# Kernel tuning notes

Hardware: AMD Instinct MI355X
Metric: run time of the kernel (lower is better)

Reference implementation:

```python
import jax, jax.numpy as jnp
import numpy as np

B, H, W, C1, C2 = 4, 256, 256, 256, 128
K = 128   # cells per patch (fixed for jit; original uses torch.unique)
E = 256   # emb_dim
NC = 16   # n_classes
G = 512   # n_genes
R = 64    # n_ref
HEADS = 8


def _w(k, shape):
    return jax.random.normal(k, shape, jnp.float32) / np.float32(np.sqrt(shape[-2]))


def setup_inputs() -> dict:
    key = jax.random.key(0)
    ks = jax.random.split(key, 20)
    return {
        "hd1": jax.random.normal(ks[0], (B, C1, H, W), jnp.float32),
        "h1": jax.random.normal(ks[1], (B, C2, H, W), jnp.float32),
        "ref_orig": jax.random.uniform(ks[2], (R, G), jnp.float32),
        "embed_w": _w(ks[3], (2 * (C1 + C2), E)),
        "comp_w1": _w(ks[4], (E, E)), "comp_w2": _w(ks[5], (E, NC)),
        "hist_w1": _w(ks[6], (E, E)), "hist_w2": _w(ks[7], (E, NC)),
        "genes_w1": _w(ks[8], (G, E)), "genes_w2": _w(ks[9], (E, NC)),
        "wref_w1": _w(ks[10], (3, E, E)), "wref_w2": _w(ks[11], (3, E, R)),
        "ca_wq": _w(ks[12], (3, NC, E)), "ca_wk": _w(ks[13], (3, G, E)),
        "ca_wv": _w(ks[14], (3, G, E)), "ca_wo": _w(ks[15], (3, E, G)),
        "nuclei_mask": jax.random.randint(ks[16], (B, H, W), 0, K + 1, jnp.int32),
        "n_cells": K,
    }


def _forward(hd1, h1, ref_orig, embed_w, comp_w1, comp_w2, hist_w1, hist_w2,
             genes_w1, genes_w2, wref_w1, wref_w2, ca_wq, ca_wk, ca_wv, ca_wo,
             nuclei_mask, n_cells):
    b, c1, hgt, wid = hd1.shape
    k_cells = n_cells
    # replaces the per-cell mask-multiply-sum loop with one segment reduce
    feat = jnp.concatenate([hd1, h1], axis=1)            # [B, C1+C2, H, W]
    cf = feat.shape[1]
    feat_flat = feat.transpose(0, 2, 3, 1).reshape(b * hgt * wid, cf)
    ids = nuclei_mask.reshape(b, hgt * wid)
    seg = jnp.where(ids > 0, jnp.arange(b)[:, None] * k_cells + ids - 1,
                    b * k_cells).reshape(-1)
    nseg = b * k_cells + 1                               # last bucket = background
    sums = jax.ops.segment_sum(feat_flat, seg, num_segments=nseg)[: b * k_cells]
    area = jax.ops.segment_sum(jnp.ones((seg.shape[0],), feat.dtype), seg,
                               num_segments=nseg)[: b * k_cells]
    cell_feat = sums / jnp.maximum(area, 1.0)[:, None]   # [N, Cf]
    glob = feat.mean((2, 3))                             # [B, Cf] = fv_hd1 ++ fv_h1
    all_fv = jnp.concatenate([cell_feat, jnp.repeat(glob, k_cells, axis=0)], axis=1)
    emb = all_fv @ embed_w                               # [N, E]
    emb_patches = emb.reshape(b, k_cells, -1).mean(1)    # per-patch mean embedding
    comp = jax.nn.softmax(jax.nn.relu(emb_patches @ comp_w1) @ comp_w2, axis=-1)
    comp_tiled = jnp.repeat(comp, k_cells, axis=0)       # [N, NC]
    out_cell_type = jax.nn.relu(emb @ hist_w1) @ hist_w2

    def branch(w1, w2, wq, wk, wv, wo):
        rw = jax.nn.softmax(jax.nn.relu(emb @ w1) @ w2, axis=-1)   # [N, R]
        ref_weighted = rw @ ref_orig                               # [N, G]
        dh = wq.shape[1] // HEADS
        q = (comp_tiled @ wq).reshape(-1, HEADS, dh)
        k = (ref_weighted @ wk).reshape(-1, HEADS, dh)
        v = (ref_weighted @ wv).reshape(-1, HEADS, dh)
        attn = jax.nn.softmax(jnp.einsum("qhd,khd->hqk", q, k) / float(np.sqrt(dh)), axis=-1)
        o = jnp.einsum("hqk,khd->qhd", attn, v).reshape(-1, HEADS * dh)
        return jax.nn.relu(ref_weighted + o @ wo)

    out_exprs = jax.vmap(branch)(wref_w1, wref_w2, ca_wq, ca_wk, ca_wv, ca_wo)  # [3,N,G]
    genes_h = jax.nn.relu(out_exprs[0] @ genes_w1)
    out_cell_type_expr = genes_h @ genes_w2
    return out_cell_type, out_exprs, out_cell_type_expr, genes_h, comp, area


def reference(hd1, h1, ref_orig, embed_w, comp_w1, comp_w2, hist_w1, hist_w2,
              genes_w1, genes_w2, wref_w1, wref_w2, ca_wq, ca_wk, ca_wv, ca_wo,
              nuclei_mask, n_cells):
    out_cell_type, out_exprs, out_cell_type_expr, genes_h, comp, area = _forward(
        hd1, h1, ref_orig, embed_w, comp_w1, comp_w2, hist_w1, hist_w2,
        genes_w1, genes_w2, wref_w1, wref_w2, ca_wq, ca_wk, ca_wv, ca_wo,
        nuclei_mask, n_cells)
    return (out_cell_type, out_exprs[0], out_exprs[1], out_exprs[2],
            out_cell_type_expr, genes_h, comp, area)
```

## Files before the change

kernel.cpp:

```cpp
#include <hip/hip_runtime.h>
#include <hip/hip_bf16.h>

#define Bn 4
#define C1n 256
#define C2n 128
#define CF 384
#define HWn 65536
#define Kc 128
#define Nn 512
#define En 256
#define NCn 16
#define Gn 512
#define Rn 64
#define HEADSn 8
#define DHn 32

#define CHK 16
#define PCH2 (HWn/CHK)
#define TC2 32
#define NT 64

#define SCALE_F 1048576.0f
#define INV_SCALE (1.0f/1048576.0f)

typedef unsigned long long ull;

__global__ void zero_k(ull* __restrict__ p, int n) {
    int i = blockIdx.x * 256 + threadIdx.x;
    if (i < n) p[i] = 0ULL;
}

__global__ __launch_bounds__(256) void area_k(const int* __restrict__ mask,
                                              int* __restrict__ area_i32) {
    int chunk = blockIdx.x, b = blockIdx.y;
    __shared__ int hist[4][129];
    int t = threadIdx.x, w = t >> 6;
    for (int i = t; i < 4 * 129; i += 256) ((int*)hist)[i] = 0;
    __syncthreads();
    const int* mp = mask + (size_t)b * HWn + chunk * PCH2;
    #pragma unroll
    for (int it = 0; it < 4; ++it) {
        int4 v = *(const int4*)(mp + it * 1024 + t * 4);
        atomicAdd(&hist[w][v.x], 1);
        atomicAdd(&hist[w][v.y], 1);
        atomicAdd(&hist[w][v.z], 1);
        atomicAdd(&hist[w][v.w], 1);
    }
    __syncthreads();
    if (t < 128) {
        int tot = hist[0][t+1] + hist[1][t+1] + hist[2][t+1] + hist[3][t+1];
        if (tot) atomicAdd(&area_i32[b * Kc + t], tot);
    }
}

__global__ __launch_bounds__(256) void segreduce3_k(
        const float* __restrict__ hd1, const float* __restrict__ h1,
        const int* __restrict__ mask,
        ull* __restrict__ sums64, ull* __restrict__ bg64) {
    int chunk = blockIdx.x, cg = blockIdx.y, b = blockIdx.z;
    int c0 = cg * TC2;
    const float* base = (c0 < C1n)
        ? hd1 + ((size_t)(b * C1n + c0)) * HWn
        : h1  + ((size_t)(b * C2n + (c0 - C1n))) * HWn;
    const int* mp = mask + (size_t)b * HWn + chunk * PCH2;

    __shared__ ull bins64[129 * TC2];
    __shared__ float tile[NT * 33];
    __shared__ __align__(16) int idsh[NT];

    int t = threadIdx.x;
    int cL = t >> 3, l8 = t & 7;
    int cA = t & 31, pg = t >> 5;
    for (int i = t; i < 129 * TC2; i += 256) bins64[i] = 0ULL;
    __syncthreads();

    for (int tl = 0; tl < PCH2 / NT; ++tl) {
        int px0 = tl * NT;
        float4 v0 = *(const float4*)(base + (size_t)cL * HWn + px0 + l8 * 4);
        float4 v1 = *(const float4*)(base + (size_t)cL * HWn + px0 + 32 + l8 * 4);
        if (t < 16) *(int4*)&idsh[t * 4] = *(const int4*)(mp + px0 + t * 4);
        int p0 = l8 * 4;
        tile[(p0 + 0) * 33 + cL] = v0.x;
        tile[(p0 + 1) * 33 + cL] = v0.y;
        tile[(p0 + 2) * 33 + cL] = v0.z;
        tile[(p0 + 3) * 33 + cL] = v0.w;
        tile[(32 + p0 + 0) * 33 + cL] = v1.x;
        tile[(32 + p0 + 1) * 33 + cL] = v1.y;
        tile[(32 + p0 + 2) * 33 + cL] = v1.z;
        tile[(32 + p0 + 3) * 33 + cL] = v1.w;
        __syncthreads();
        #pragma unroll
        for (int pp = 0; pp < 8; ++pp) {
            int p = pg * 8 + pp;
            int id = idsh[p];
            float v = tile[p * 33 + cA];
            long long qv = __float2ll_rn(v * SCALE_F);
            atomicAdd(&bins64[id * TC2 + cA], (ull)qv);
        }
        __syncthreads();
    }
    for (int i = t; i < 129 * TC2; i += 256) {
        int cell = i >> 5, cc = i & 31;
        ull v = bins64[i];
        if (v) {
            if (cell == 0) atomicAdd(&bg64[b * CF + c0 + cc], v);
            else atomicAdd(&sums64[((size_t)(b * Kc + cell - 1)) * CF + c0 + cc], v);
        }
    }
}

__global__ void glob_k(const ull* __restrict__ sums64, const ull* __restrict__ bg64,
                       const int* __restrict__ area_i32, float* __restrict__ glob,
                       float* __restrict__ areaf, float* __restrict__ area_out) {
    int idx = blockIdx.x * 256 + threadIdx.x;
    if (idx < Bn * CF) {
        int b = idx / CF, c = idx - b * CF;
        long long s = (long long)bg64[idx];
        for (int cell = 0; cell < Kc; ++cell)
            s += (long long)sums64[((size_t)(b * Kc + cell)) * CF + c];
        glob[idx] = (float)s * (INV_SCALE / (float)HWn);
    }
    if (idx < Nn) {
        float a = (float)area_i32[idx];
        areaf[idx] = a;
        area_out[idx] = a;
    }
}

__global__ __launch_bounds__(256) void gemm_emb_k(
        const ull* __restrict__ sums64, const float* __restrict__ glob,
        const float* __restrict__ areaf, const float* __restrict__ Bw,
        float* __restrict__ C) {
    int row0 = blockIdx.x * 2;
    __shared__ float As[2 * 768];
    __shared__ float part[2048];
    __shared__ float rina[2];
    int t = threadIdx.x, lane = t & 63, w = t >> 6;
    if (t < 2) rina[t] = 1.f / fmaxf(areaf[row0 + t], 1.f);
    __syncthreads();
    for (int idx = t; idx < 2 * 768; idx += 256) {
        int r = idx / 768, k = idx - r * 768;
        int row = row0 + r;
        float v;
        if (k < CF) v = (float)(long long)sums64[(size_t)row * CF + k] * INV_SCALE * rina[r];
        else        v = glob[(row >> 7) * CF + (k - CF)];
        As[idx] = v;
    }
    __syncthreads();
    float acc[2][4] = {{0,0,0,0},{0,0,0,0}};
    const int KQ = 192;
    const float* bp = Bw + (size_t)(w * KQ) * 256 + lane * 4;
    #pragma unroll 8
    for (int k = 0; k < KQ; ++k) {
        float4 bv = *(const float4*)(bp + (size_t)k * 256);
        float a0 = As[w * KQ + k], a1 = As[768 + w * KQ + k];
        acc[0][0] = fmaf(a0, bv.x, acc[0][0]); acc[0][1] = fmaf(a0, bv.y, acc[0][1]);
        acc[0][2] = fmaf(a0, bv.z, acc[0][2]); acc[0][3] = fmaf(a0, bv.w, acc[0][3]);
        acc[1][0] = fmaf(a1, bv.x, acc[1][0]); acc[1][1] = fmaf(a1, bv.y, acc[1][1]);
        acc[1][2] = fmaf(a1, bv.z, acc[1][2]); acc[1][3] = fmaf(a1, bv.w, acc[1][3]);
    }
    *(float4*)&part[(w * 2 + 0) * 256 + lane * 4] = make_float4(acc[0][0], acc[0][1], acc[0][2], acc[0][3]);
    *(float4*)&part[(w * 2 + 1) * 256 + lane * 4] = make_float4(acc[1][0], acc[1][1], acc[1][2], acc[1][3]);
    __syncthreads();
    #pragma unroll
    for (int i2 = 0; i2 < 2; ++i2) {
        int idx = i2 * 256 + t, r = idx >> 8, c = idx & 255;
        float s = part[r*256+c] + part[(2+r)*256+c] + part[(4+r)*256+c] + part[(6+r)*256+c];
        C[(size_t)(row0 + r) * En + c] = s;
    }
}

__global__ void patch_mean_k(const float* __restrict__ emb, float* __restrict__ ep) {
    int b = blockIdx.x, j = threadIdx.x;
    float s = 0.f;
    for (int r = 0; r < Kc; r++) s += emb[(size_t)(b * Kc + r) * En + j];
    ep[b * En + j] = s * (1.f / (float)Kc);
}

__global__ void comp_mlp_k(const float* __restrict__ ep, const float* __restrict__ w1,
                           const float* __restrict__ w2, float* __restrict__ comp_ws,
                           float* __restrict__ comp_out) {
    int b = blockIdx.x, j = threadIdx.x;
    __shared__ float h[En];
    __shared__ float c[NCn];
    float acc = 0.f;
    #pragma unroll 8
    for (int k = 0; k < En; k++) acc = fmaf(ep[b * En + k], w1[(size_t)k * En + j], acc);
    h[j] = fmaxf(acc, 0.f);
    __syncthreads();
    if (j < NCn) {
        float a2 = 0.f;
        #pragma unroll 8
        for (int k = 0; k < En; k++) a2 = fmaf(h[k], w2[(size_t)k * NCn + j], a2);
        c[j] = a2;
    }
    __syncthreads();
    if (j == 0) {
        float m = c[0];
        for (int q = 1; q < NCn; q++) m = fmaxf(m, c[q]);
        float s = 0.f;
        for (int q = 0; q < NCn; q++) { c[q] = __expf(c[q] - m); s += c[q]; }
        float inv = 1.f / s;
        for (int q = 0; q < NCn; q++) c[q] *= inv;
    }
    __syncthreads();
    if (j < NCn) {
        comp_ws[b * NCn + j] = c[j];
        comp_out[b * NCn + j] = c[j];
    }
}

__global__ __launch_bounds__(256) void fused_hist_k(
        const float* __restrict__ emb, const float* __restrict__ w1,
        const float* __restrict__ w2, float* __restrict__ out) {
    int row0 = blockIdx.x * 2;
    __shared__ float As[2 * En];
    __shared__ float part[2048];
    __shared__ float Hs[2 * En];
    int t = threadIdx.x, lane = t & 63, w = t >> 6;
    if (t < 128) *(float4*)&As[t * 4] = *(const float4*)(emb + (size_t)row0 * En + t * 4);
    __syncthreads();
    float acc[2][4] = {{0,0,0,0},{0,0,0,0}};
    const float* bp = w1 + (size_t)(w * 64) * 256 + lane * 4;
    #pragma unroll 8
    for (int k = 0; k < 64; ++k) {
        float4 bv = *(const float4*)(bp + (size_t)k * 256);
        float a0 = As[w * 64 + k], a1 = As[256 + w * 64 + k];
        acc[0][0] = fmaf(a0, bv.x, acc[0][0]); acc[0][1] = fmaf(a0, bv.y, acc[0][1]);
        acc[0][2] = fmaf(a0, bv.z, acc[0][2]); acc[0][3] = fmaf(a0, bv.w, acc[0][3]);
        acc[1][0] = fmaf(a1, bv.x, acc[1][0]); acc[1][1] = fmaf(a1, bv.y, acc[1][1]);
        acc[1][2] = fmaf(a1, bv.z, acc[1][2]); acc[1][3] = fmaf(a1, bv.w, acc[1][3]);
    }
    *(float4*)&part[(w * 2 + 0) * 256 + lane * 4] = make_float4(acc[0][0], acc[0][1], acc[0][2], acc[0][3]);
    *(float4*)&part[(w * 2 + 1) * 256 + lane * 4] = make_float4(acc[1][0], acc[1][1], acc[1][2], acc[1][3]);
    __syncthreads();
    #pragma unroll
    for (int i2 = 0; i2 < 2; ++i2) {
        int idx = i2 * 256 + t, r = idx >> 8, c = idx & 255;
        float s = part[r*256+c] + part[(2+r)*256+c] + part[(4+r)*256+c] + part[(6+r)*256+c];
        Hs[r * 256 + c] = fmaxf(s, 0.f);
    }
    __syncthreads();
    if (t < 32) {
        int r = t >> 4, j = t & 15;
        float a2 = 0.f;
        #pragma unroll 8
        for (int k = 0; k < En; k++) a2 = fmaf(Hs[r * 256 + k], w2[(size_t)k * NCn + j], a2);
        out[(size_t)(row0 + r) * NCn + j] = a2;
    }
}

__global__ __launch_bounds__(256) void fused_branch_k(
        const float* __restrict__ emb, const float* __restrict__ wref_w1,
        const float* __restrict__ wref_w2, const float* __restrict__ ref,
        float* __restrict__ refw) {
    int i = blockIdx.y, row0 = blockIdx.x * 2;
    const float* w1 = wref_w1 + (size_t)i * En * En;
    const float* w2 = wref_w2 + (size_t)i * En * Rn;
    __shared__ float As[2 * En];
    __shared__ float part[2048];
    __shared__ float Hs[2 * En];
    __shared__ float RW[2 * Rn];
    int t = threadIdx.x, lane = t & 63, w = t >> 6;
    if (t < 128) *(float4*)&As[t * 4] = *(const float4*)(emb + (size_t)row0 * En + t * 4);
    __syncthreads();
    {
        float acc[2][4] = {{0,0,0,0},{0,0,0,0}};
        const float* bp = w1 + (size_t)(w * 64) * 256 + lane * 4;
        #pragma unroll 8
        for (int k = 0; k < 64; ++k) {
            float4 bv = *(const float4*)(bp + (size_t)k * 256);
            float a0 = As[w * 64 + k], a1 = As[256 + w * 64 + k];
            acc[0][0] = fmaf(a0, bv.x, acc[0][0]); acc[0][1] = fmaf(a0, bv.y, acc[0][1]);
            acc[0][2] = fmaf(a0, bv.z, acc[0][2]); acc[0][3] = fmaf(a0, bv.w, acc[0][3]);
            acc[1][0] = fmaf(a1, bv.x, acc[1][0]); acc[1][1] = fmaf(a1, bv.y, acc[1][1]);
            acc[1][2] = fmaf(a1, bv.z, acc[1][2]); acc[1][3] = fmaf(a1, bv.w, acc[1][3]);
        }
        *(float4*)&part[(w * 2 + 0) * 256 + lane * 4] = make_float4(acc[0][0], acc[0][1], acc[0][2], acc[0][3]);
        *(float4*)&part[(w * 2 + 1) * 256 + lane * 4] = make_float4(acc[1][0], acc[1][1], acc[1][2], acc[1][3]);
    }
    __syncthreads();
    #pragma unroll
    for (int i2 = 0; i2 < 2; ++i2) {
        int idx = i2 * 256 + t, r = idx >> 8, c = idx & 255;
        float s = part[r*256+c] + part[(2+r)*256+c] + part[(4+r)*256+c] + part[(6+r)*256+c];
        Hs[r * 256 + c] = fmaxf(s, 0.f);
    }
    __syncthreads();
    {
        float a0 = 0.f, a1 = 0.f;
        const float* bp = w2 + (size_t)(w * 64) * 64 + lane;
        #pragma unroll 8
        for (int k = 0; k < 64; ++k) {
            float bv = bp[(size_t)k * 64];
            a0 = fmaf(Hs[w * 64 + k], bv, a0);
            a1 = fmaf(Hs[256 + w * 64 + k], bv, a1);
        }
        part[(w * 2 + 0) * 64 + lane] = a0;
        part[(w * 2 + 1) * 64 + lane] = a1;
    }
    __syncthreads();
    if (t < 128) {
        int r = t >> 6, c = t & 63;
        RW[r * 64 + c] = part[r*64+c] + part[(2+r)*64+c] + part[(4+r)*64+c] + part[(6+r)*64+c];
    }
    __syncthreads();
    if (w < 2) {
        float v = RW[w * 64 + lane];
        float m = v;
        #pragma unroll
        for (int o = 32; o > 0; o >>= 1) m = fmaxf(m, __shfl_xor(m, o));
        float e = __expf(v - m), s = e;
        #pragma unroll
        for (int o = 32; o > 0; o >>= 1) s += __shfl_xor(s, o);
        RW[w * 64 + lane] = e / s;
    }
    __syncthreads();
    {
        int q = t & 127, kh = t >> 7;
        float acc[2][4] = {{0,0,0,0},{0,0,0,0}};
        const float* bp = ref + (size_t)(kh * 32) * 512 + q * 4;
        #pragma unroll 8
        for (int k = 0; k < 32; ++k) {
            float4 bv = *(const float4*)(bp + (size_t)k * 512);
            float a0 = RW[kh * 32 + k], a1 = RW[64 + kh * 32 + k];
            acc[0][0] = fmaf(a0, bv.x, acc[0][0]); acc[0][1] = fmaf(a0, bv.y, acc[0][1]);
            acc[0][2] = fmaf(a0, bv.z, acc[0][2]); acc[0][3] = fmaf(a0, bv.w, acc[0][3]);
            acc[1][0] = fmaf(a1, bv.x, acc[1][0]); acc[1][1] = fmaf(a1, bv.y, acc[1][1]);
            acc[1][2] = fmaf(a1, bv.z, acc[1][2]); acc[1][3] = fmaf(a1, bv.w, acc[1][3]);
        }
        *(float4*)&part[(kh * 2 + 0) * 512 + q * 4] = make_float4(acc[0][0], acc[0][1], acc[0][2], acc[0][3]);
        *(float4*)&part[(kh * 2 + 1) * 512 + q * 4] = make_float4(acc[1][0], acc[1][1], acc[1][2], acc[1][3]);
    }
    __syncthreads();
    float* op = refw + ((size_t)i * Nn + row0) * Gn;
    #pragma unroll
    for (int i2 = 0; i2 < 4; ++i2) {
        int idx = i2 * 256 + t, r = idx >> 9, c = idx & 511;
        op[(size_t)r * Gn + c] = part[r * 512 + c] + part[(2 + r) * 512 + c];
    }
}

__global__ __launch_bounds__(256) void fused_kv_k(
        const float* __restrict__ refw, const float* __restrict__ ca_wk,
        const float* __restrict__ ca_wv, float* __restrict__ kws,
        float* __restrict__ vws) {
    int i = blockIdx.y, row0 = blockIdx.x * 2;
    const float* wk = ca_wk + (size_t)i * Gn * En;
    const float* wv = ca_wv + (size_t)i * Gn * En;
    __shared__ float As[2 * Gn];
    __shared__ float part[2048];
    int t = threadIdx.x, lane = t & 63, w = t >> 6;
    const float* rp = refw + ((size_t)i * Nn + row0) * Gn;
    *(float4*)&As[t * 4] = *(const float4*)(rp + t * 4);
    __syncthreads();
    int which = w >> 1, half = w & 1;
    const float* Bp = (which ? wv : wk) + (size_t)(half * 256) * En + lane * 4;
    float acc[2][4] = {{0,0,0,0},{0,0,0,0}};
    #pragma unroll 8
    for (int k = 0; k < 256; ++k) {
        float4 bv = *(const float4*)(Bp + (size_t)k * En);
        float a0 = As[half * 256 + k], a1 = As[512 + half * 256 + k];
        acc[0][0] = fmaf(a0, bv.x, acc[0][0]); acc[0][1] = fmaf(a0, bv.y, acc[0][1]);
        acc[0][2] = fmaf(a0, bv.z, acc[0][2]); acc[0][3] = fmaf(a0, bv.w, acc[0][3]);
        acc[1][0] = fmaf(a1, bv.x, acc[1][0]); acc[1][1] = fmaf(a1, bv.y, acc[1][1]);
        acc[1][2] = fmaf(a1, bv.z, acc[1][2]); acc[1][3] = fmaf(a1, bv.w, acc[1][3]);
    }
    *(float4*)&part[(w * 2 + 0) * 256 + lane * 4] = make_float4(acc[0][0], acc[0][1], acc[0][2], acc[0][3]);
    *(float4*)&part[(w * 2 + 1) * 256 + lane * 4] = make_float4(acc[1][0], acc[1][1], acc[1][2], acc[1][3]);
    __syncthreads();
    #pragma unroll
    for (int i2 = 0; i2 < 2; ++i2) {
        int idx = i2 * 256 + t, r = idx >> 8, c = idx & 255;
        float sk = part[r * 256 + c] + part[(2 + r) * 256 + c];
        float sv = part[(4 + r) * 256 + c] + part[(6 + r) * 256 + c];
        kws[((size_t)i * Nn + row0 + r) * En + c] = sk;
        vws[((size_t)i * Nn + row0 + r) * En + c] = sv;
    }
}

template <int R, bool RELU>
__global__ void gemm_rows_k(const float* __restrict__ A, long long sA,
                            const float* __restrict__ Bw, long long sB,
                            float* __restrict__ C, long long sC,
                            int M, int N, int K) {
    int i = blockIdx.y;
    A += (size_t)i * sA; Bw += (size_t)i * sB; C += (size_t)i * sC;
    int row0 = blockIdx.x * R;
    extern __shared__ float As[];
    for (int idx = threadIdx.x; idx < R * K; idx += blockDim.x)
        As[idx] = A[(size_t)(row0 + idx / K) * K + (idx % K)];
    __syncthreads();
    for (int j = threadIdx.x; j < N; j += blockDim.x) {
        float acc[R];
        #pragma unroll
        for (int r = 0; r < R; r++) acc[r] = 0.f;
        const float* bp = Bw + j;
        #pragma unroll 8
        for (int k = 0; k < K; k++) {
            float bv = bp[(size_t)k * N];
            #pragma unroll
            for (int r = 0; r < R; r++) acc[r] = fmaf(As[r * K + k], bv, acc[r]);
        }
        #pragma unroll
        for (int r = 0; r < R; r++) {
            float v = acc[r];
            if (RELU) v = fmaxf(v, 0.f);
            C[(size_t)(row0 + r) * N + j] = v;
        }
    }
}

__global__ __launch_bounds__(256) void attn_k(
        const float* __restrict__ compw, const float* __restrict__ wq,
        const float* __restrict__ kmat, const float* __restrict__ vmat,
        float* __restrict__ o4) {
    int i = blockIdx.y, b = blockIdx.x & 3, h = blockIdx.x >> 2;
    const float* wqi = wq + (size_t)i * NCn * En;
    const float* km = kmat + (size_t)i * Nn * En;
    const float* vm = vmat + (size_t)i * Nn * En;
    __shared__ float q[DHn];
    __shared__ float p[Nn];
    __shared__ float red[4];
    __shared__ float pvp[8][33];
    int t = threadIdx.x;
    if (t < DHn) {
        float acc = 0.f;
        #pragma unroll
        for (int c = 0; c < NCn; c++)
            acc = fmaf(compw[b * NCn + c], wqi[(size_t)c * En + h * DHn + t], acc);
        q[t] = acc;
    }
    __syncthreads();
    const float scale = 0.17677669529663687f;
    float sv0, sv1;
    {
        const float* kr = km + (size_t)t * En + h * DHn;
        float a = 0.f;
        #pragma unroll
        for (int d = 0; d < DHn; d++) a = fmaf(q[d], kr[d], a);
        sv0 = a * scale;
        kr += (size_t)256 * En;
        a = 0.f;
        #pragma unroll
        for (int d = 0; d < DHn; d++) a = fmaf(q[d], kr[d], a);
        sv1 = a * scale;
    }
    float lm = fmaxf(sv0, sv1);
    #pragma unroll
    for (int o = 32; o > 0; o >>= 1) lm = fmaxf(lm, __shfl_xor(lm, o));
    if ((t & 63) == 0) red[t >> 6] = lm;
    __syncthreads();
    float m = fmaxf(fmaxf(red[0], red[1]), fmaxf(red[2], red[3]));
    __syncthreads();
    float e0 = __expf(sv0 - m), e1 = __expf(sv1 - m);
    p[t] = e0; p[t + 256] = e1;
    float ls = e0 + e1;
    #pragma unroll
    for (int o = 32; o > 0; o >>= 1) ls += __shfl_xor(ls, o);
    if ((t & 63) == 0) red[t >> 6] = ls;
    __syncthreads();
    float ssum = red[0] + red[1] + red[2] + red[3];
    int d = t & 31, seg = t >> 5;
    float acc = 0.f;
    const float* vp = vm + (size_t)(seg * 64) * En + h * DHn + d;
    #pragma unroll 8
    for (int j = 0; j < 64; ++j) acc = fmaf(p[seg * 64 + j], vp[(size_t)j * En], acc);
    pvp[seg][d] = acc;
    __syncthreads();
    if (t < DHn) {
        float o = 0.f;
        #pragma unroll
        for (int s8 = 0; s8 < 8; ++s8) o += pvp[s8][t];
        o4[((size_t)i * Bn + b) * En + h * DHn + t] = o / ssum;
    }
}

__global__ void add_relu_k(const float* __restrict__ refw, const float* __restrict__ ow,
                           float* __restrict__ out) {
    int i = blockIdx.y, n = blockIdx.x, b = n >> 7;
    const float4* rr = (const float4*)(refw + ((size_t)i * Nn + n) * Gn);
    const float4* oo = (const float4*)(ow + ((size_t)i * Bn + b) * Gn);
    float4* op = (float4*)(out + (size_t)i * (Nn * Gn) + (size_t)n * Gn);
    int j = threadIdx.x;
    float4 a = rr[j], o = oo[j];
    op[j] = make_float4(fmaxf(a.x + o.x, 0.f), fmaxf(a.y + o.y, 0.f),
                        fmaxf(a.z + o.z, 0.f), fmaxf(a.w + o.w, 0.f));
}

__global__ __launch_bounds__(256) void fused_genes_k(
        const float* __restrict__ e0, const float* __restrict__ gw1,
        const float* __restrict__ gw2, float* __restrict__ gh,
        float* __restrict__ octe) {
    int row0 = blockIdx.x * 2;
    __shared__ float As[2 * Gn];
    __shared__ float part[2048];
    __shared__ float Hs[2 * En];
    int t = threadIdx.x, lane = t & 63, w = t >> 6;
    *(float4*)&As[t * 4] = *(const float4*)(e0 + (size_t)row0 * Gn + t * 4);
    __syncthreads();
    {
        float acc[2][4] = {{0,0,0,0},{0,0,0,0}};
        const float* bp = gw1 + (size_t)(w * 128) * 256 + lane * 4;
        #pragma unroll 8
        for (int k = 0; k < 128; ++k) {
            float4 bv = *(const float4*)(bp + (size_t)k * 256);
            float a0 = As[w * 128 + k], a1 = As[512 + w * 128 + k];
            acc[0][0] = fmaf(a0, bv.x, acc[0][0]); acc[0][1] = fmaf(a0, bv.y, acc[0][1]);
            acc[0][2] = fmaf(a0, bv.z, acc[0][2]); acc[0][3] = fmaf(a0, bv.w, acc[0][3]);
            acc[1][0] = fmaf(a1, bv.x, acc[1][0]); acc[1][1] = fmaf(a1, bv.y, acc[1][1]);
            acc[1][2] = fmaf(a1, bv.z, acc[1][2]); acc[1][3] = fmaf(a1, bv.w, acc[1][3]);
        }
        *(float4*)&part[(w * 2 + 0) * 256 + lane * 4] = make_float4(acc[0][0], acc[0][1], acc[0][2], acc[0][3]);
        *(float4*)&part[(w * 2 + 1) * 256 + lane * 4] = make_float4(acc[1][0], acc[1][1], acc[1][2], acc[1][3]);
    }
    __syncthreads();
    #pragma unroll
    for (int i2 = 0; i2 < 2; ++i2) {
        int idx = i2 * 256 + t, r = idx >> 8, c = idx & 255;
        float s = part[r*256+c] + part[(2+r)*256+c] + part[(4+r)*256+c] + part[(6+r)*256+c];
        float v = fmaxf(s, 0.f);
        Hs[r * 256 + c] = v;
        gh[(size_t)(row0 + r) * En + c] = v;
    }
    __syncthreads();
    if (t < 32) {
        int r = t >> 4, j = t & 15;
        float a2 = 0.f;
        #pragma unroll 8
        for (int k = 0; k < En; k++) a2 = fmaf(Hs[r * 256 + k], gw2[(size_t)k * NCn + j], a2);
        octe[(size_t)(row0 + r) * NCn + j] = a2;
    }
}

extern "C" void kernel_launch(void* const* d_in, const int* in_sizes, int n_in,
                              void* d_out, int out_size, void* d_ws, size_t ws_size,
                              hipStream_t stream) {
    const float* hd1     = (const float*)d_in[0];
    const float* h1      = (const float*)d_in[1];
    const float* ref     = (const float*)d_in[2];
    const float* embed_w = (const float*)d_in[3];
    const float* comp_w1 = (const float*)d_in[4];
    const float* comp_w2 = (const float*)d_in[5];
    const float* hist_w1 = (const float*)d_in[6];
    const float* hist_w2 = (const float*)d_in[7];
    const float* genes_w1= (const float*)d_in[8];
    const float* genes_w2= (const float*)d_in[9];
    const float* wref_w1 = (const float*)d_in[10];
    const float* wref_w2 = (const float*)d_in[11];
    const float* ca_wq   = (const float*)d_in[12];
    const float* ca_wk   = (const float*)d_in[13];
    const float* ca_wv   = (const float*)d_in[14];
    const float* ca_wo   = (const float*)d_in[15];
    const int*   mask    = (const int*)d_in[16];

    float* out = (float*)d_out;
    const size_t o_ct   = 0;
    const size_t o_e0   = 8192;
    const size_t o_octe = 8192 + 3 * 262144;
    const size_t o_gh   = o_octe + 8192;
    const size_t o_comp = o_gh + 131072;
    const size_t o_area = o_comp + 64;

    ull* sums64 = (ull*)d_ws;
    ull* bg64   = sums64 + 196608;
    int* area_i32 = (int*)(bg64 + 1536);
    float* fbase = (float*)(sums64 + 196608 + 1536 + 256);
    float* glob  = fbase;
    float* areaf = glob + 1536;
    float* emb   = areaf + 512;
    float* ep    = emb + 131072;
    float* compw = ep + 1024;
    float* refw  = compw + 64;
    float* kws   = refw + 786432;
    float* vws   = kws + 393216;
    float* o4    = vws + 393216;
    float* ow    = o4 + 3072;

    const int nzero = 196608 + 1536 + 256;
    zero_k<<<(nzero + 255) / 256, 256, 0, stream>>>(sums64, nzero);
    area_k<<<dim3(CHK, Bn), 256, 0, stream>>>(mask, area_i32);
    segreduce3_k<<<dim3(CHK, CF / TC2, Bn), 256, 0, stream>>>(hd1, h1, mask, sums64, bg64);
    glob_k<<<6, 256, 0, stream>>>(sums64, bg64, area_i32, glob, areaf, out + o_area);
    gemm_emb_k<<<Nn / 2, 256, 0, stream>>>(sums64, glob, areaf, embed_w, emb);
    patch_mean_k<<<Bn, 256, 0, stream>>>(emb, ep);
    comp_mlp_k<<<Bn, 256, 0, stream>>>(ep, comp_w1, comp_w2, compw, out + o_comp);

    fused_hist_k<<<Nn / 2, 256, 0, stream>>>(emb, hist_w1, hist_w2, out + o_ct);
    fused_branch_k<<<dim3(Nn / 2, 3), 256, 0, stream>>>(emb, wref_w1, wref_w2, ref, refw);
    fused_kv_k<<<dim3(Nn / 2, 3), 256, 0, stream>>>(refw, ca_wk, ca_wv, kws, vws);
    attn_k<<<dim3(HEADSn * Bn, 3), 256, 0, stream>>>(compw, ca_wq, kws, vws, o4);
    gemm_rows_k<4, false><<<dim3(1, 3), 256, 4 * 256 * 4, stream>>>(
        o4, (long long)Bn * En, ca_wo, (long long)En * Gn, ow, (long long)Bn * Gn, Bn, Gn, En);
    add_relu_k<<<dim3(Nn, 3), 128, 0, stream>>>(refw, ow, out + o_e0);

    fused_genes_k<<<Nn / 2, 256, 0, stream>>>(out + o_e0, genes_w1, genes_w2,
                                              out + o_gh, out + o_octe);
}
```

Before: 711.6 us.

## Replace global 64-bit atomics with per-chunk int32 partials and a reduce pass

```diff
diff --git a/kernel.cpp b/kernel.cpp
--- a/kernel.cpp
+++ b/kernel.cpp
@@ -15,7 +15,7 @@
 #define HEADSn 8
 #define DHn 32
 
-#define CHK 16
+#define CHK 32
 #define PCH2 (HWn/CHK)
 #define TC2 32
 #define NT 64
@@ -25,13 +25,8 @@
 
 typedef unsigned long long ull;
 
-__global__ void zero_k(ull* __restrict__ p, int n) {
-    int i = blockIdx.x * 256 + threadIdx.x;
-    if (i < n) p[i] = 0ULL;
-}
-
 __global__ __launch_bounds__(256) void area_k(const int* __restrict__ mask,
-                                              int* __restrict__ area_i32) {
+                                              int* __restrict__ apart) {
     int chunk = blockIdx.x, b = blockIdx.y;
     __shared__ int hist[4][129];
     int t = threadIdx.x, w = t >> 6;
@@ -39,7 +34,7 @@
     __syncthreads();
     const int* mp = mask + (size_t)b * HWn + chunk * PCH2;
     #pragma unroll
-    for (int it = 0; it < 4; ++it) {
+    for (int it = 0; it < PCH2 / 1024; ++it) {
         int4 v = *(const int4*)(mp + it * 1024 + t * 4);
         atomicAdd(&hist[w][v.x], 1);
         atomicAdd(&hist[w][v.y], 1);
@@ -47,16 +42,15 @@
         atomicAdd(&hist[w][v.w], 1);
     }
     __syncthreads();
-    if (t < 128) {
-        int tot = hist[0][t+1] + hist[1][t+1] + hist[2][t+1] + hist[3][t+1];
-        if (tot) atomicAdd(&area_i32[b * Kc + t], tot);
-    }
+    if (t < 128)
+        apart[(chunk * Bn + b) * Kc + t] =
+            hist[0][t+1] + hist[1][t+1] + hist[2][t+1] + hist[3][t+1];
 }
 
 __global__ __launch_bounds__(256) void segreduce3_k(
         const float* __restrict__ hd1, const float* __restrict__ h1,
         const int* __restrict__ mask,
-        ull* __restrict__ sums64, ull* __restrict__ bg64) {
+        int* __restrict__ spart) {
     int chunk = blockIdx.x, cg = blockIdx.y, b = blockIdx.z;
     int c0 = cg * TC2;
     const float* base = (c0 < C1n)
@@ -64,14 +58,14 @@
         : h1  + ((size_t)(b * C2n + (c0 - C1n))) * HWn;
     const int* mp = mask + (size_t)b * HWn + chunk * PCH2;
 
-    __shared__ ull bins64[129 * TC2];
+    __shared__ int bins[129 * TC2];
     __shared__ float tile[NT * 33];
     __shared__ __align__(16) int idsh[NT];
 
     int t = threadIdx.x;
     int cL = t >> 3, l8 = t & 7;
     int cA = t & 31, pg = t >> 5;
-    for (int i = t; i < 129 * TC2; i += 256) bins64[i] = 0ULL;
+    for (int i = t; i < 129 * TC2; i += 256) bins[i] = 0;
     __syncthreads();
 
     for (int tl = 0; tl < PCH2 / NT; ++tl) {
@@ -94,41 +88,54 @@
             int p = pg * 8 + pp;
             int id = idsh[p];
             float v = tile[p * 33 + cA];
-            long long qv = __float2ll_rn(v * SCALE_F);
-            atomicAdd(&bins64[id * TC2 + cA], (ull)qv);
+            int qv = __float2int_rn(v * SCALE_F);
+            atomicAdd(&bins[id * TC2 + cA], qv);
         }
         __syncthreads();
     }
     for (int i = t; i < 129 * TC2; i += 256) {
         int cell = i >> 5, cc = i & 31;
-        ull v = bins64[i];
-        if (v) {
-            if (cell == 0) atomicAdd(&bg64[b * CF + c0 + cc], v);
-            else atomicAdd(&sums64[((size_t)(b * Kc + cell - 1)) * CF + c0 + cc], v);
-        }
-    }
-}
-
-__global__ void glob_k(const ull* __restrict__ sums64, const ull* __restrict__ bg64,
-                       const int* __restrict__ area_i32, float* __restrict__ glob,
+        spart[((size_t)(chunk * Bn + b) * 129 + cell) * CF + c0 + cc] = bins[i];
+    }
+}
+
+__global__ void reduce_k(const int* __restrict__ spart, float* __restrict__ ctot) {
+    int idx = blockIdx.x * 256 + threadIdx.x;
+    if (idx >= Bn * 129 * CF) return;
+    int b = idx / (129 * CF);
+    int rem = idx - b * 129 * CF;
+    long long s = 0;
+    #pragma unroll 8
+    for (int ch = 0; ch < CHK; ++ch)
+        s += spart[((size_t)ch * Bn + b) * (129 * CF) + rem];
+    ctot[idx] = (float)s * INV_SCALE;
+}
+
+__global__ void glob_k(const float* __restrict__ ctot, const int* __restrict__ apart,
+                       float* __restrict__ glob,
                        float* __restrict__ areaf, float* __restrict__ area_out) {
     int idx = blockIdx.x * 256 + threadIdx.x;
     if (idx < Bn * CF) {
         int b = idx / CF, c = idx - b * CF;
-        long long s = (long long)bg64[idx];
-        for (int cell = 0; cell < Kc; ++cell)
-            s += (long long)sums64[((size_t)(b * Kc + cell)) * CF + c];
-        glob[idx] = (float)s * (INV_SCALE / (float)HWn);
+        float s = 0.f;
+        for (int cell = 0; cell < 129; ++cell)
+            s += ctot[((size_t)(b * 129 + cell)) * CF + c];
+        glob[idx] = s * (1.0f / (float)HWn);
     }
     if (idx < Nn) {
-        float a = (float)area_i32[idx];
+        int b = idx >> 7, cell = idx & 127;
+        int s = 0;
+        #pragma unroll 8
+        for (int ch = 0; ch < CHK; ++ch)
+            s += apart[(ch * Bn + b) * Kc + cell];
+        float a = (float)s;
         areaf[idx] = a;
         area_out[idx] = a;
     }
 }
 
 __global__ __launch_bounds__(256) void gemm_emb_k(
-        const ull* __restrict__ sums64, const float* __restrict__ glob,
+        const float* __restrict__ ctot, const float* __restrict__ glob,
         const float* __restrict__ areaf, const float* __restrict__ Bw,
         float* __restrict__ C) {
     int row0 = blockIdx.x * 2;
@@ -142,8 +149,12 @@
         int r = idx / 768, k = idx - r * 768;
         int row = row0 + r;
         float v;
-        if (k < CF) v = (float)(long long)sums64[(size_t)row * CF + k] * INV_SCALE * rina[r];
-        else        v = glob[(row >> 7) * CF + (k - CF)];
+        if (k < CF) {
+            int bb = row >> 7, cell = (row & 127) + 1;
+            v = ctot[((size_t)(bb * 129 + cell)) * CF + k] * rina[r];
+        } else {
+            v = glob[(row >> 7) * CF + (k - CF)];
+        }
         As[idx] = v;
     }
     __syncthreads();
@@ -562,11 +573,10 @@
     const size_t o_comp = o_gh + 131072;
     const size_t o_area = o_comp + 64;
 
-    ull* sums64 = (ull*)d_ws;
-    ull* bg64   = sums64 + 196608;
-    int* area_i32 = (int*)(bg64 + 1536);
-    float* fbase = (float*)(sums64 + 196608 + 1536 + 256);
-    float* glob  = fbase;
+    int*  spart = (int*)d_ws;
+    int*  apart = spart + (size_t)CHK * Bn * 129 * CF;
+    float* ctot = (float*)(apart + CHK * Bn * Kc);
+    float* glob = ctot + Bn * 129 * CF;
     float* areaf = glob + 1536;
     float* emb   = areaf + 512;
     float* ep    = emb + 131072;
@@ -577,12 +587,11 @@
     float* o4    = vws + 393216;
     float* ow    = o4 + 3072;
 
-    const int nzero = 196608 + 1536 + 256;
-    zero_k<<<(nzero + 255) / 256, 256, 0, stream>>>(sums64, nzero);
-    area_k<<<dim3(CHK, Bn), 256, 0, stream>>>(mask, area_i32);
-    segreduce3_k<<<dim3(CHK, CF / TC2, Bn), 256, 0, stream>>>(hd1, h1, mask, sums64, bg64);
-    glob_k<<<6, 256, 0, stream>>>(sums64, bg64, area_i32, glob, areaf, out + o_area);
-    gemm_emb_k<<<Nn / 2, 256, 0, stream>>>(sums64, glob, areaf, embed_w, emb);
+    area_k<<<dim3(CHK, Bn), 256, 0, stream>>>(mask, apart);
+    segreduce3_k<<<dim3(CHK, CF / TC2, Bn), 256, 0, stream>>>(hd1, h1, mask, spart);
+    reduce_k<<<(Bn * 129 * CF + 255) / 256, 256, 0, stream>>>(spart, ctot);
+    glob_k<<<6, 256, 0, stream>>>(ctot, apart, glob, areaf, out + o_area);
+    gemm_emb_k<<<Nn / 2, 256, 0, stream>>>(ctot, glob, areaf, embed_w, emb);
     patch_mean_k<<<Bn, 256, 0, stream>>>(emb, ep);
     comp_mlp_k<<<Bn, 256, 0, stream>>>(ep, comp_w1, comp_w2, compw, out + o_comp);
 
```

Result: faster. 657.0 us (-7.7%).
